# Optimization experiments

Hardware: AMD Instinct MI355X
Metric: run time of the kernel (lower is better)

Reference implementation:

```python
import jax, jax.numpy as jnp
import numpy as np

KSIZE = 3
SCALE = 10.0
EPS = 1e-4


def _prelu(x, a):
    return jnp.where(x >= 0, x, a * x)


def _conv1x1(x, w, b):
    # x: [B,C,H,W], w: [O,C], b: [O]
    return jnp.einsum('bchw,oc->bohw', x, w) + b[None, :, None, None]


def _extract_patches(x, k):
    # same-padded kxk patches, torch-unfold channel-major ordering.
    # x: [B,C,H,W] -> [B, H*W, C, k, k]
    B, C, H, W = x.shape
    p = k // 2
    xp = jnp.pad(x, ((0, 0), (0, 0), (p, p), (p, p)))
    pats = jnp.stack([xp[:, :, i:i + H, j:j + W]
                      for i in range(k) for j in range(k)], axis=2)  # [B,C,k*k,H,W]
    pats = pats.reshape(B, C, k, k, H * W)
    return jnp.transpose(pats, (0, 4, 1, 2, 3))


def setup_inputs() -> dict:
    key = jax.random.key(0)
    ks = jax.random.split(key, 10)
    B, C, r = 4, 64, 2
    H = W = 96
    h = w = 48
    Cr = C // r
    s = 0.05
    return {
        'input': jax.random.normal(ks[0], (B, C, H, W), jnp.float32),
        'small': jax.random.normal(ks[1], (B, C, h, w), jnp.float32),
        'w_match1': jax.random.normal(ks[2], (Cr, C), jnp.float32) * s,
        'b_match1': jax.random.normal(ks[3], (Cr,), jnp.float32) * s,
        'a_match1': jnp.full((1,), 0.25, jnp.float32),
        'w_match2': jax.random.normal(ks[4], (Cr, C), jnp.float32) * s,
        'b_match2': jax.random.normal(ks[5], (Cr,), jnp.float32) * s,
        'a_match2': jnp.full((1,), 0.25, jnp.float32),
        'w_asm': jax.random.normal(ks[6], (C, C), jnp.float32) * s,
        'b_asm': jax.random.normal(ks[7], (C,), jnp.float32) * s,
        'a_asm': jnp.full((1,), 0.25, jnp.float32),
    }


def reference(input, small, w_match1, b_match1, a_match1,
              w_match2, b_match2, a_match2, w_asm, b_asm, a_asm):
    dn = ('NCHW', 'OIHW', 'NCHW')
    pad1 = [(1, 1), (1, 1)]

    match_input = _prelu(_conv1x1(input, w_match1, b_match1), a_match1)  # [B,Cr,H,W]
    embed_w = _prelu(_conv1x1(small, w_asm, b_asm), a_asm)               # [B,C,h,w]
    ref = _prelu(_conv1x1(small, w_match2, b_match2), a_match2)          # [B,Cr,h,w]

    raw_w = _extract_patches(embed_w, KSIZE)  # [B, L, C, 3, 3]  (reconstruction filters)
    w_pat = _extract_patches(ref, KSIZE)      # [B, L, Cr, 3, 3] (matching filters)

    def per_sample(xi, wi, raw_wi):
        # xi: [Cr,H,W], wi: [L,Cr,3,3], raw_wi: [L,C,3,3]
        norm = jnp.sqrt(jnp.sum(wi * wi, axis=(1, 2, 3), keepdims=True))
        wi_n = wi / jnp.maximum(norm, EPS)
        # dynamic conv: correlation of xi with all L normalized patches
        yi = jax.lax.conv_general_dilated(xi[None], wi_n, (1, 1), pad1,
                                          dimension_numbers=dn)  # [1,L,H,W]
        yi = jax.nn.softmax(yi * SCALE, axis=1)
        # conv_transpose2d(yi, raw_wi, stride=2, padding=1):
        # lhs_dilation=2, pad k-1-p=1, spatially flipped, in/out swapped kernel
        wt = jnp.transpose(raw_wi, (1, 0, 2, 3))[:, :, ::-1, ::-1]  # [C,L,3,3]
        out = jax.lax.conv_general_dilated(yi, wt, (1, 1), pad1,
                                           lhs_dilation=(2, 2),
                                           dimension_numbers=dn)  # [1,C,2H-1,2W-1]
        return out[0] / 6.0

    return jax.vmap(per_sample)(match_input, w_pat, raw_w)
```

## Files before the change

kernel.cpp:

```cpp
#include <hip/hip_runtime.h>


typedef unsigned short u16;
typedef __attribute__((ext_vector_type(8))) short short8;
typedef __attribute__((ext_vector_type(8))) _Float16 half8;
typedef __attribute__((ext_vector_type(4))) float f32x4;

__device__ __forceinline__ u16 f2bf(float f) {
    unsigned u = __float_as_uint(f);
    unsigned r = (u + 0x7FFFu + ((u >> 16) & 1u)) >> 16;
    return (u16)r;
}
__device__ __forceinline__ float bf2f(u16 h) {
    return __uint_as_float(((unsigned)h) << 16);
}
__device__ __forceinline__ u16 f2h(float f) {
    _Float16 h = (_Float16)f;
    u16 u; __builtin_memcpy(&u, &h, 2); return u;
}
__device__ __forceinline__ float h2f(u16 u) {
    _Float16 h; __builtin_memcpy(&h, &u, 2); return (float)h;
}

__global__ void kzero(float4* p, long n) {
    long i = (long)blockIdx.x * blockDim.x + threadIdx.x;
    long st = (long)gridDim.x * blockDim.x;
    float4 z; z.x = 0.f; z.y = 0.f; z.z = 0.f; z.w = 0.f;
    for (; i < n; i += st) p[i] = z;
}

__global__ void kmatch(const float* __restrict__ input, const float* __restrict__ w1,
                       const float* __restrict__ b1, const float* __restrict__ a1,
                       u16* __restrict__ xf16) {
    __shared__ float xl[64 * 96];
    __shared__ float wl[32 * 65];
    int b = blockIdx.x / 96, y = blockIdx.x % 96;
    int tid = threadIdx.x;
    for (int i = tid; i < 64 * 96; i += 256) {
        int ci = i / 96, xx = i % 96;
        xl[i] = input[(((b * 64 + ci) * 96) + y) * 96 + xx];
    }
    for (int i = tid; i < 2048; i += 256) wl[(i >> 6) * 65 + (i & 63)] = w1[i];
    __syncthreads();
    float aa = a1[0];
    for (int o = tid; o < 96 * 32; o += 256) {
        int xx = o >> 5, c = o & 31;
        float acc = b1[c];
        #pragma unroll
        for (int ci = 0; ci < 64; ci++) acc = fmaf(xl[ci * 96 + xx], wl[c * 65 + ci], acc);
        float v = acc >= 0.f ? acc : aa * acc;
        xf16[((b * 98 + y + 1) * 98 + (xx + 1)) * 32 + c] = f2h(v);
    }
}

__global__ void ksmall(const float* __restrict__ small, const float* __restrict__ wasm,
                       const float* __restrict__ basm, const float* __restrict__ aasm,
                       const float* __restrict__ wm2, const float* __restrict__ bm2,
                       const float* __restrict__ am2,
                       float* __restrict__ ef32, u16* __restrict__ rkl) {
    __shared__ float sl[64 * 48];
    __shared__ float wa[64 * 65];
    __shared__ float wm[32 * 65];
    int b = blockIdx.x / 48, y = blockIdx.x % 48;
    int tid = threadIdx.x;
    for (int i = tid; i < 64 * 48; i += 256) {
        int ci = i / 48, xx = i % 48;
        sl[i] = small[(((b * 64 + ci) * 48) + y) * 48 + xx];
    }
    for (int i = tid; i < 4096; i += 256) wa[(i >> 6) * 65 + (i & 63)] = wasm[i];
    for (int i = tid; i < 2048; i += 256) wm[(i >> 6) * 65 + (i & 63)] = wm2[i];
    __syncthreads();
    float ae = aasm[0], ar = am2[0];
    for (int o = tid; o < 48 * 64; o += 256) {
        int xx = o >> 6, c = o & 63;
        float acc = basm[c];
        #pragma unroll
        for (int ci = 0; ci < 64; ci++) acc = fmaf(sl[ci * 48 + xx], wa[c * 65 + ci], acc);
        float v = acc >= 0.f ? acc : ae * acc;
        ef32[((b * 50 + y + 1) * 50 + (xx + 1)) * 64 + c] = v;
    }
    for (int o = tid; o < 48 * 32; o += 256) {
        int xx = o >> 5, c = o & 31;
        float acc = bm2[c];
        #pragma unroll
        for (int ci = 0; ci < 64; ci++) acc = fmaf(sl[ci * 48 + xx], wm[c * 65 + ci], acc);
        float v = acc >= 0.f ? acc : ar * acc;
        rkl[((b * 50 + y + 1) * 50 + (xx + 1)) * 32 + c] = f2h(v);
    }
}

__global__ void kinvnorm(const u16* __restrict__ rkl, float* __restrict__ invn) {
    int idx = blockIdx.x * 256 + threadIdx.x;
    int b = idx / 2304, l = idx % 2304;
    int ly = l / 48, lx = l % 48;
    float s = 0.f;
    for (int ty = 0; ty < 3; ty++)
        for (int tx = 0; tx < 3; tx++) {
            int base = ((b * 50 + ly + ty) * 50 + (lx + tx)) * 32;
            #pragma unroll
            for (int c = 0; c < 32; c++) {
                float v = h2f(rkl[base + c]);
                s = fmaf(v, v, s);
            }
        }
    invn[idx] = 10.f / fmaxf(sqrtf(s), 1e-4f);
}

__global__ void kvtp(const float* __restrict__ ef32, u16* __restrict__ vtp) {
    __shared__ float el[3][50 * 64];
    int bi = blockIdx.x;
    int b = bi / 48, ly = bi % 48;
    const float* eb = ef32 + (size_t)b * 50 * 50 * 64;
    int tid = threadIdx.x;
    #pragma unroll
    for (int r = 0; r < 3; ++r)
        for (int i = tid; i < 800; i += 256)
            ((float4*)el[r])[i] = ((const float4*)(eb + (size_t)(ly + r) * 3200))[i];
    __syncthreads();
    u16* vo = vtp + (size_t)b * 576 * 2304 + (size_t)ly * 48;
    for (int n = tid; n < 576; n += 256) {
        int t = n >> 6, c = n & 63;
        int ty = t / 3, tx = t - ty * 3;
        u16* dst = vo + (size_t)n * 2304;
        const float* src = &el[ty][tx * 64 + c];
        #pragma unroll
        for (int g = 0; g < 12; ++g) {
            unsigned lo = (unsigned)f2bf(src[(g * 4 + 0) * 64]) |
                          ((unsigned)f2bf(src[(g * 4 + 1) * 64]) << 16);
            unsigned hi = (unsigned)f2bf(src[(g * 4 + 2) * 64]) |
                          ((unsigned)f2bf(src[(g * 4 + 3) * 64]) << 16);
            uint2 pk; pk.x = lo; pk.y = hi;
            *(uint2*)&dst[g * 4] = pk;
        }
    }
}

__device__ __forceinline__ void stage_ks(const u16* __restrict__ src, u16* dst, int tid) {
    int wb = tid & ~63;
    #pragma unroll
    for (int k = 0; k < 3; ++k)
        __builtin_amdgcn_global_load_lds(
            (const __attribute__((address_space(1))) void*)(src + (size_t)(tid + k * 256) * 8),
            (__attribute__((address_space(3))) void*)(dst + (size_t)(wb + k * 256) * 8),
            16, 0, 0);
    if (tid < 32)
        __builtin_amdgcn_global_load_lds(
            (const __attribute__((address_space(1))) void*)(src + (size_t)(tid + 768) * 8),
            (__attribute__((address_space(3))) void*)(dst + (size_t)768 * 8),
            16, 0, 0);
}

__launch_bounds__(256, 2)
__global__ void kfused3(const u16* __restrict__ xf16, const u16* __restrict__ rkl,
                        const u16* __restrict__ vtp, const float* __restrict__ invn,
                        float* __restrict__ Z, int b0, int nb) {
    __shared__ u16 Ks[2][6400];
    __shared__ u16 Pl[2][6144];
    __shared__ float Ln[2304];
    __shared__ u16 Qs[6 * 18 * 32];
    __shared__ float llds[4][16];

    int tid = threadIdx.x;
    int w = tid >> 6, lane = tid & 63, l15 = lane & 15, quad = lane >> 4;
    int bi = blockIdx.x, brel, t;
    if (nb == 4) { brel = bi & 3; t = bi >> 2; }
    else         { brel = 0; t = bi; }
    int b = b0 + brel;
    int px0 = (t % 6) * 16, pyb = (t / 6) * 4;

    const u16* xb = xf16 + (size_t)b * 98 * 98 * 32;
    const u16* rb = rkl + (size_t)b * 50 * 50 * 32;
    const float* invb = invn + b * 2304;
    const u16* vw = vtp + (size_t)b * 576 * 2304 + (size_t)(w * 144 + l15) * 2304 + quad * 8;

    stage_ks(rb, Ks[0], tid);
    __builtin_amdgcn_sched_barrier(0);

    for (int i = tid; i < 576; i += 256)
        ((float4*)Ln)[i] = ((const float4*)invb)[i];

    for (int u = tid; u < 432; u += 256) {
        int cell = u >> 2, ch = u & 3;
        int r = cell / 18, p = cell % 18;
        *(short8*)&Qs[(r * 18 + p) * 32 + ch * 8] =
            *(const short8*)(xb + (((pyb + r) * 98) + (px0 + p)) * 32 + ch * 8);
    }

    f32x4 acc[36];
    #pragma unroll
    for (int i = 0; i < 36; i++) acc[i] = (f32x4)0.f;
    float lacc[4] = {0.f, 0.f, 0.f, 0.f};

    __syncthreads();

    short8 vv[9];

    for (int it = 0; it < 24; ++it) {
        int ly0 = it * 2;
        int cur = it & 1;

        if (it < 23) stage_ks(rb + (ly0 + 2) * 1600, Ks[cur ^ 1], tid);
        __builtin_amdgcn_sched_barrier(0x38F);

        const u16* vit = vw + it * 96;
        #pragma unroll
        for (int nt = 0; nt < 9; ++nt) vv[nt] = *(const short8*)(vit + (size_t)nt * 36864);

        const u16* Kc = Ks[cur];
        u16* Pc = Pl[cur];
        #pragma unroll
        for (int kh = 0; kh < 2; ++kh) {
            f32x4 sf[3];
            #pragma unroll
            for (int i = 0; i < 3; i++) sf[i] = (f32x4)0.f;
            __builtin_amdgcn_s_setprio(1);
            #pragma unroll
            for (int ty = 0; ty < 3; ++ty)
                #pragma unroll
                for (int tx = 0; tx < 3; ++tx) {
                    half8 a = *(const half8*)&Qs[((w + ty) * 18 + (l15 + tx)) * 32 + quad * 8];
                    #pragma unroll
                    for (int lxo = 0; lxo < 3; ++lxo) {
                        half8 bb = *(const half8*)&Kc[(kh + ty) * 1600 + (lxo * 16 + l15 + tx) * 32 + quad * 8];
                        sf[lxo] = __builtin_amdgcn_mfma_f32_16x16x32_f16(a, bb, sf[lxo], 0, 0, 0);
                    }
                }
            __builtin_amdgcn_s_setprio(0);
            #pragma unroll
            for (int lxo = 0; lxo < 3; ++lxo) {
                float invs = Ln[(ly0 + kh) * 48 + lxo * 16 + l15];
                int k = kh * 48 + lxo * 16 + l15;
                int kb = k >> 5;
                int kc = (k & 31) ^ (quad << 3);
                #pragma unroll
                for (int r = 0; r < 4; ++r) {
                    float p = __expf(sf[lxo][r] * invs);
                    u16 h = f2bf(p);
                    Pc[(w * 3 + kb) * 512 + (quad * 4 + r) * 32 + kc] = h;
                    lacc[r] += bf2f(h);
                }
            }
        }

        asm volatile("s_waitcnt vmcnt(9) lgkmcnt(0)" ::: "memory");
        __builtin_amdgcn_s_barrier();
        __builtin_amdgcn_sched_barrier(0);

        const u16* Pr = Pl[cur];
        int pcol = l15 * 32 + ((quad ^ (l15 >> 2)) & 3) * 8;
        __builtin_amdgcn_s_setprio(1);
        #pragma unroll
        for (int ks = 0; ks < 3; ++ks) {
            short8 pa0 = *(const short8*)&Pr[(0 * 3 + ks) * 512 + pcol];
            short8 pa1 = *(const short8*)&Pr[(1 * 3 + ks) * 512 + pcol];
            #pragma unroll
            for (int nt = 0; nt < 9; ++nt) {
                short8 vn = vv[nt];
                acc[0 * 9 + nt] = __builtin_amdgcn_mfma_f32_16x16x32_bf16(pa0, vn, acc[0 * 9 + nt], 0, 0, 0);
                acc[1 * 9 + nt] = __builtin_amdgcn_mfma_f32_16x16x32_bf16(pa1, vn, acc[1 * 9 + nt], 0, 0, 0);
            }
            pa0 = *(const short8*)&Pr[(2 * 3 + ks) * 512 + pcol];
            pa1 = *(const short8*)&Pr[(3 * 3 + ks) * 512 + pcol];
            #pragma unroll
            for (int nt = 0; nt < 9; ++nt) {
                short8 vn = vv[nt];
                acc[2 * 9 + nt] = __builtin_amdgcn_mfma_f32_16x16x32_bf16(pa0, vn, acc[2 * 9 + nt], 0, 0, 0);
                acc[3 * 9 + nt] = __builtin_amdgcn_mfma_f32_16x16x32_bf16(pa1, vn, acc[3 * 9 + nt], 0, 0, 0);
                if (ks < 2)
                    vv[nt] = *(const short8*)(vit + (size_t)nt * 36864 + (ks + 1) * 32);
            }
        }
        __builtin_amdgcn_s_setprio(0);
    }

    #pragma unroll
    for (int r = 0; r < 4; ++r) {
        float v = lacc[r];
        v += __shfl_xor(v, 1);
        v += __shfl_xor(v, 2);
        v += __shfl_xor(v, 4);
        v += __shfl_xor(v, 8);
        lacc[r] = v;
    }
    if (l15 == 0) {
        #pragma unroll
        for (int r = 0; r < 4; ++r)
            llds[w][quad * 4 + r] = lacc[r];
    }
    __syncthreads();
    float* Zb = Z + (size_t)brel * 9216 * 576;
    #pragma unroll
    for (int mt = 0; mt < 4; ++mt) {
        #pragma unroll
        for (int r = 0; r < 4; ++r) {
            int q = (pyb + mt) * 96 + px0 + quad * 4 + r;
            float rl = 1.0f / (llds[mt][quad * 4 + r] * 6.0f);
            float* zr = Zb + (size_t)q * 576 + w * 144;
            #pragma unroll
            for (int nt = 0; nt < 9; ++nt)
                __builtin_nontemporal_store(acc[mt * 9 + nt][r] * rl, zr + nt * 16 + l15);
        }
    }
}

__global__ void kgather(const float* __restrict__ Z, float* __restrict__ out, int b0) {
    __shared__ float zb[2 * 9 * 580];
    int bi = blockIdx.x;
    int brel = bi / (96 * 12);
    int rem = bi % (96 * 12);
    int b = b0 + brel;
    int q = rem / 12, xt = rem % 12;
    int ox0 = xt * 16, p0 = ox0 >> 1;
    const float* Zb = Z + (size_t)brel * 9216 * 576;
    int tid = threadIdx.x;
    for (int id = tid; id < 2592; id += 256) {
        int pi = id / 1296, r2 = id % 1296;
        int pxi = r2 / 144, n4 = r2 % 144;
        int py = q + pi; if (py > 95) py = 95;
        int px = p0 + pxi; if (px > 95) px = 95;
        *(float4*)&zb[(pi * 9 + pxi) * 580 + n4 * 4] =
            *(const float4*)&Zb[(size_t)(py * 96 + px) * 576 + n4 * 4];
    }
    __syncthreads();
    int xi = tid & 15, cq = tid >> 4;
    int ox = ox0 + xi;
    bool oxv = ox <= 190;
    int ntx, txl[2], pxl[2];
    if (xi & 1) { ntx = 2; txl[0] = 0; pxl[0] = (xi + 1) >> 1; txl[1] = 2; pxl[1] = (xi - 1) >> 1; }
    else        { ntx = 1; txl[0] = 1; pxl[0] = xi >> 1; txl[1] = 1; pxl[1] = xi >> 1; }
    int oy0 = 2 * q;
    #pragma unroll
    for (int ck = 0; ck < 4; ++ck) {
        int c = cq + ck * 16;
        float v0 = 0.f, v1 = 0.f;
        for (int j = 0; j < ntx; ++j) {
            int tx = txl[j], pxi = pxl[j];
            v0 += zb[(0 * 9 + pxi) * 580 + (3 + tx) * 64 + c];
            v1 += zb[(1 * 9 + pxi) * 580 + (0 + tx) * 64 + c];
            v1 += zb[(0 * 9 + pxi) * 580 + (6 + tx) * 64 + c];
        }
        if (oxv) {
            float* o = out + (((size_t)(b * 64 + c) * 191 + oy0) * 191 + ox);
            *o = v0;
            if (q < 95) *(o + 191) = v1;
        }
    }
}

extern "C" void kernel_launch(void* const* d_in, const int* in_sizes, int n_in,
                              void* d_out, int out_size, void* d_ws, size_t ws_size,
                              hipStream_t stream) {
    const float* input = (const float*)d_in[0];
    const float* small = (const float*)d_in[1];
    const float* w1 = (const float*)d_in[2];
    const float* b1 = (const float*)d_in[3];
    const float* a1 = (const float*)d_in[4];
    const float* w2 = (const float*)d_in[5];
    const float* b2 = (const float*)d_in[6];
    const float* a2 = (const float*)d_in[7];
    const float* wa = (const float*)d_in[8];
    const float* ba = (const float*)d_in[9];
    const float* aa = (const float*)d_in[10];

    char* ws = (char*)d_ws;
    u16* xf16 = (u16*)(ws + 0);
    u16* rkl = (u16*)(ws + 2458624);
    float* ef = (float*)(ws + 3098624);
    u16* vtp = (u16*)(ws + 5658624);
    float* invn = (float*)(ws + 16275456);
    const size_t PREP = 16312320;
    float* Zbuf = (float*)(ws + PREP);
    float* out = (float*)d_out;

    int nb = (ws_size >= (size_t)101246976) ? 4 : 1;

    kzero<<<1024, 256, 0, stream>>>((float4*)ws, 5658624 / 16);
    kmatch<<<384, 256, 0, stream>>>(input, w1, b1, a1, xf16);
    ksmall<<<192, 256, 0, stream>>>(small, wa, ba, aa, w2, b2, a2, ef, rkl);
    kinvnorm<<<36, 256, 0, stream>>>(rkl, invn);
    kvtp<<<192, 256, 0, stream>>>(ef, vtp);

    for (int b0 = 0; b0 < 4; b0 += nb) {
        kfused3<<<nb * 144, 256, 0, stream>>>(xf16, rkl, vtp, invn, Zbuf, b0, nb);
        kgather<<<nb * 1152, 256, 0, stream>>>(Zbuf, out, b0);
    }
}
```

Baseline: 528.8 us.

## Use ring buffer of K rows to stage only two new rows per iteration

```diff
diff --git a/kernel.cpp b/kernel.cpp
--- a/kernel.cpp
+++ b/kernel.cpp
@@ -135,7 +135,7 @@
     }
 }
 
-__device__ __forceinline__ void stage_ks(const u16* __restrict__ src, u16* dst, int tid) {
+__device__ __forceinline__ void stage_ks4(const u16* __restrict__ src, u16* dst, int tid) {
     int wb = tid & ~63;
     #pragma unroll
     for (int k = 0; k < 3; ++k)
@@ -149,14 +149,25 @@
             (__attribute__((address_space(3))) void*)(dst + (size_t)768 * 8),
             16, 0, 0);
 }
+__device__ __forceinline__ void stage_ks2(const u16* __restrict__ src, u16* dst, int tid) {
+    int wb = tid & ~63;
+    __builtin_amdgcn_global_load_lds(
+        (const __attribute__((address_space(1))) void*)(src + (size_t)tid * 8),
+        (__attribute__((address_space(3))) void*)(dst + (size_t)wb * 8),
+        16, 0, 0);
+    if (tid < 144)
+        __builtin_amdgcn_global_load_lds(
+            (const __attribute__((address_space(1))) void*)(src + (size_t)(tid + 256) * 8),
+            (__attribute__((address_space(3))) void*)(dst + (size_t)(wb + 256) * 8),
+            16, 0, 0);
+}
 
 __launch_bounds__(256, 2)
 __global__ void kfused3(const u16* __restrict__ xf16, const u16* __restrict__ rkl,
                         const u16* __restrict__ vtp, const float* __restrict__ invn,
                         float* __restrict__ Z, int b0, int nb) {
-    __shared__ u16 Ks[2][6400];
+    __shared__ u16 Ks[6][1600];
     __shared__ u16 Pl[2][6144];
-    __shared__ float Ln[2304];
     __shared__ u16 Qs[6 * 18 * 32];
     __shared__ float llds[4][16];
 
@@ -173,11 +184,8 @@
     const float* invb = invn + b * 2304;
     const u16* vw = vtp + (size_t)b * 576 * 2304 + (size_t)(w * 144 + l15) * 2304 + quad * 8;
 
-    stage_ks(rb, Ks[0], tid);
+    stage_ks4(rb, &Ks[0][0], tid);
     __builtin_amdgcn_sched_barrier(0);
-
-    for (int i = tid; i < 576; i += 256)
-        ((float4*)Ln)[i] = ((const float4*)invb)[i];
 
     for (int u = tid; u < 432; u += 256) {
         int cell = u >> 2, ch = u & 3;
@@ -194,19 +202,29 @@
     __syncthreads();
 
     short8 vv[9];
+    int s0 = 0;
 
     for (int it = 0; it < 24; ++it) {
         int ly0 = it * 2;
         int cur = it & 1;
 
-        if (it < 23) stage_ks(rb + (ly0 + 2) * 1600, Ks[cur ^ 1], tid);
+        float pinv[2][3];
+        #pragma unroll
+        for (int kh = 0; kh < 2; ++kh)
+            #pragma unroll
+            for (int lxo = 0; lxo < 3; ++lxo)
+                pinv[kh][lxo] = invb[(ly0 + kh) * 48 + lxo * 16 + l15];
+
+        if (it < 23) {
+            int s4 = s0 + 4; if (s4 >= 6) s4 -= 6;
+            stage_ks2(rb + (size_t)(ly0 + 4) * 1600, &Ks[0][0] + s4 * 1600, tid);
+        }
         __builtin_amdgcn_sched_barrier(0x38F);
 
         const u16* vit = vw + it * 96;
         #pragma unroll
         for (int nt = 0; nt < 9; ++nt) vv[nt] = *(const short8*)(vit + (size_t)nt * 36864);
 
-        const u16* Kc = Ks[cur];
         u16* Pc = Pl[cur];
         #pragma unroll
         for (int kh = 0; kh < 2; ++kh) {
@@ -215,20 +233,23 @@
             for (int i = 0; i < 3; i++) sf[i] = (f32x4)0.f;
             __builtin_amdgcn_s_setprio(1);
             #pragma unroll
-            for (int ty = 0; ty < 3; ++ty)
+            for (int ty = 0; ty < 3; ++ty) {
+                int rr = s0 + kh + ty; if (rr >= 6) rr -= 6;
+                const u16* Kr = &Ks[0][0] + rr * 1600;
                 #pragma unroll
                 for (int tx = 0; tx < 3; ++tx) {
                     half8 a = *(const half8*)&Qs[((w + ty) * 18 + (l15 + tx)) * 32 + quad * 8];
                     #pragma unroll
                     for (int lxo = 0; lxo < 3; ++lxo) {
-                        half8 bb = *(const half8*)&Kc[(kh + ty) * 1600 + (lxo * 16 + l15 + tx) * 32 + quad * 8];
+                        half8 bb = *(const half8*)&Kr[(lxo * 16 + l15 + tx) * 32 + quad * 8];
                         sf[lxo] = __builtin_amdgcn_mfma_f32_16x16x32_f16(a, bb, sf[lxo], 0, 0, 0);
                     }
                 }
+            }
             __builtin_amdgcn_s_setprio(0);
             #pragma unroll
             for (int lxo = 0; lxo < 3; ++lxo) {
-                float invs = Ln[(ly0 + kh) * 48 + lxo * 16 + l15];
+                float invs = pinv[kh][lxo];
                 int k = kh * 48 + lxo * 16 + l15;
                 int kb = k >> 5;
                 int kc = (k & 31) ^ (quad << 3);
@@ -271,6 +292,8 @@
             }
         }
         __builtin_amdgcn_s_setprio(0);
+
+        s0 += 2; if (s0 >= 6) s0 -= 6;
     }
 
     #pragma unroll
```

Measured after the change: 490.7 us. -7.2%, faster.
